# Performance work log

Measured on AMD Instinct MI355X. Metric: run time of the kernel, lower is better.

Reference implementation:

```python
import jax, jax.numpy as jnp
import numpy as np
import math

D, NH, NL, NP = 256, 8, 3, 4
HD = D // NH
SPATIAL = ((128, 128), (64, 64), (32, 32))  # static value_spatial_shapes, one (h,w) per level


def _offset_bias():
    # replicates _reset_parameters grid init for sampling_offsets.bias
    thetas = jnp.arange(NH, dtype=jnp.float32) * (2.0 * math.pi / NH)
    grid = jnp.stack([jnp.cos(thetas), jnp.sin(thetas)], -1)  # (NH, 2)
    grid = grid[:, None, None, :] * (jnp.arange(NP, dtype=jnp.float32) + 1.0)[None, None, :, None]
    return jnp.broadcast_to(grid, (NH, NL, NP, 2)).reshape(-1)  # (NH*NL*NP*2,)


def setup_inputs() -> dict:
    key = jax.random.key(0)
    k = jax.random.split(key, 7)
    bs, Lq = 4, 8192
    Lv = sum(h * w for h, w in SPATIAL)  # 21504
    s = 0.02
    return {
        "query": jax.random.normal(k[0], (bs, Lq, D), jnp.float32),
        "reference_points": jax.random.uniform(k[1], (bs, Lq, 4), jnp.float32),
        "value": jax.random.normal(k[2], (bs, Lv, D), jnp.float32),
        "W_off": jax.random.normal(k[3], (D, NH * NL * NP * 2), jnp.float32) * 0.001,
        "b_off": _offset_bias(),
        "W_attn": jax.random.normal(k[4], (D, NH * NL * NP), jnp.float32) * s,
        "b_attn": jnp.zeros((NH * NL * NP,), jnp.float32),
        "W_v": jax.random.normal(k[5], (D, D), jnp.float32) * s,
        "b_v": jnp.zeros((D,), jnp.float32),
        "W_out": jax.random.normal(k[6], (D, D), jnp.float32) * s,
        "b_out": jnp.zeros((D,), jnp.float32),
    }


def _bilinear(vflat, h, w, gx, gy):
    # F.grid_sample(mode='bilinear', align_corners=False, padding_mode='zeros')
    # vflat: (B, C, h*w); gx, gy: (B, P) in [-1, 1] -> (B, C, P)
    x = ((gx + 1.0) * w - 1.0) * 0.5
    y = ((gy + 1.0) * h - 1.0) * 0.5
    x0f = jnp.floor(x); y0f = jnp.floor(y)
    wx1 = x - x0f; wy1 = y - y0f
    x0 = x0f.astype(jnp.int32); y0 = y0f.astype(jnp.int32)

    def gather(xi, yi, wgt):
        valid = (xi >= 0) & (xi < w) & (yi >= 0) & (yi < h)
        idx = jnp.clip(yi, 0, h - 1) * w + jnp.clip(xi, 0, w - 1)
        g = jnp.take_along_axis(vflat, idx[:, None, :], axis=2)  # (B, C, P)
        return g * (wgt * valid)[:, None, :]

    return (gather(x0, y0, (1.0 - wx1) * (1.0 - wy1))
            + gather(x0 + 1, y0, wx1 * (1.0 - wy1))
            + gather(x0, y0 + 1, (1.0 - wx1) * wy1)
            + gather(x0 + 1, y0 + 1, wx1 * wy1))


def reference(query, reference_points, value, W_off, b_off, W_attn, b_attn, W_v, b_v, W_out, b_out):
    bs, Lq, _ = query.shape
    v = value @ W_v + b_v                                           # (bs, Lv, D)
    v4 = v.reshape(bs, -1, NH, HD)
    off = (query @ W_off + b_off).reshape(bs, Lq, NH, NL, NP, 2)
    aw = jax.nn.softmax((query @ W_attn + b_attn).reshape(bs, Lq, NH, NL * NP), axis=-1)
    aw = aw.reshape(bs, Lq, NH, NL, NP)
    ref = reference_points[..., :2][:, :, None, None, None, :]      # (bs, Lq, 1, 1, 1, 2)
    pts = jnp.clip(ref + off, 0.0, 1.0)                             # (bs, Lq, NH, NL, NP, 2)

    out = jnp.zeros((bs, Lq, NH, HD), query.dtype)
    start = 0
    for lvl, (h, w) in enumerate(SPATIAL):
        # faithful to torch source: (bs, NH, h*w, HD) reinterpreted row-major as (bs*NH, HD, h, w)
        v_lvl = v4[:, start:start + h * w].transpose(0, 2, 1, 3).reshape(bs * NH, HD, h * w)
        g = pts[:, :, :, lvl].transpose(0, 2, 1, 3, 4).reshape(bs * NH, Lq * NP, 2) * 2.0 - 1.0
        sampled = _bilinear(v_lvl, h, w, g[..., 0], g[..., 1]).reshape(bs, NH, HD, Lq, NP)
        out = out + jnp.einsum('bhdqp,bhqp->bqhd', sampled, aw[:, :, :, lvl].transpose(0, 2, 1, 3))
        start += h * w

    return out.reshape(bs, Lq, D) @ W_out + b_out
```

## Files before the change

kernel.cpp:

```cpp
#include <hip/hip_runtime.h>
#include <math.h>

#define LV 21504
#define LQ 8192
#define BS 4
#define NHD 8
#define HD 32
#define DIM 256

typedef __attribute__((ext_vector_type(4))) float f32x4;
typedef __attribute__((ext_vector_type(8))) short s16x8;
typedef unsigned short ushort_t;
typedef unsigned int uint_t;

__device__ __forceinline__ void bsplit(float f, ushort_t& h, ushort_t& l) {
  uint_t u = __float_as_uint(f);
  uint_t hr = (u + 0x7fffu + ((u >> 16) & 1u)) >> 16;
  h = (ushort_t)hr;
  float fh = __uint_as_float(hr << 16);
  float fl = f - fh;
  uint_t v = __float_as_uint(fl);
  l = (ushort_t)((v + 0x7fffu + ((v >> 16) & 1u)) >> 16);
}

__device__ __forceinline__ uint_t bf16rne(float f) {
  uint_t u = __float_as_uint(f);
  return (u + 0x7fffu + ((u >> 16) & 1u)) >> 16;
}

__global__ __launch_bounds__(256) void k_wsplit(
    const float* __restrict__ Wv, const float* __restrict__ Woff,
    const float* __restrict__ Wattn, ushort_t* __restrict__ wbuf)
{
  int c = blockIdx.x;
  int k = threadIdx.x;
  float w;
  ushort_t *dh, *dl;
  if (c < 256) {
    w = Wv[(size_t)k * 256 + c];
    dh = wbuf + (size_t)c * 256 + k;
    dl = wbuf + 65536 + (size_t)c * 256 + k;
  } else {
    int co = c - 256;
    w = (co < 192) ? Woff[(size_t)k * 192 + co] : Wattn[(size_t)k * 96 + (co - 192)];
    dh = wbuf + 131072 + (size_t)co * 256 + k;
    dl = wbuf + 204800 + (size_t)co * 256 + k;
  }
  ushort_t h, l;
  bsplit(w, h, l);
  *dh = h; *dl = l;
}

__global__ __launch_bounds__(256) void k_wsplit2(
    const float* __restrict__ Wout, ushort_t* __restrict__ tb)
{
  int c = blockIdx.x;
  int k = threadIdx.x;
  float w = Wout[(size_t)k * 256 + c];
  ushort_t h, l;
  bsplit(w, h, l);
  tb[(size_t)c * 256 + k] = h;
  tb[65536 + (size_t)c * 256 + k] = l;
}

__global__ __launch_bounds__(256, 3) void k_vproj(
    const float* __restrict__ value, const ushort_t* __restrict__ wbuf,
    const float* __restrict__ bv, ushort_t* __restrict__ vvb)
{
  __shared__ ushort_t lA[2][2][64][72];

  int bid = blockIdx.x;
  int b = bid / 336, rem = bid % 336;
  int l, mp;
  if (rem < 256)      { l = 0; mp = rem; }
  else if (rem < 320) { l = 1; mp = rem - 256; }
  else                { l = 2; mp = rem - 320; }
  const int startl[3] = {0, 16384, 20480};
  const int hwd[3]    = {512, 128, 32};
  int start = startl[l], hd32 = hwd[l], m0 = mp * 2;

  int t = threadIdx.x;
  int wave = t >> 6, lane = t & 63;
  int l15 = lane & 15, l4 = lane >> 4;
  int n0 = wave * 64;

  const float* Ab = value + (size_t)b * LV * DIM;
  int r0s = t >> 4, kq = t & 15;
  const float* aptr[4];
  #pragma unroll
  for (int j = 0; j < 4; ++j) {
    int row = r0s + 16 * j;
    aptr[j] = Ab + (size_t)(start + (row & 31) * hd32 + m0 + (row >> 5)) * DIM + kq * 4;
  }

  f32x4 acc[4][4];
  #pragma unroll
  for (int m = 0; m < 4; ++m)
    #pragma unroll
    for (int n = 0; n < 4; ++n) acc[m][n] = (f32x4){0.f, 0.f, 0.f, 0.f};

  float4 pf[4];
  #pragma unroll
  for (int j = 0; j < 4; ++j) pf[j] = *(const float4*)(aptr[j]);

  #pragma unroll
  for (int j = 0; j < 4; ++j) {
    int row = r0s + 16 * j;
    float a[4] = {pf[j].x, pf[j].y, pf[j].z, pf[j].w};
    ushort_t hh[4], ll[4];
    #pragma unroll
    for (int q = 0; q < 4; ++q) bsplit(a[q], hh[q], ll[q]);
    uint2 uh, ul;
    uh.x = (uint_t)hh[0] | ((uint_t)hh[1] << 16);
    uh.y = (uint_t)hh[2] | ((uint_t)hh[3] << 16);
    ul.x = (uint_t)ll[0] | ((uint_t)ll[1] << 16);
    ul.y = (uint_t)ll[2] | ((uint_t)ll[3] << 16);
    *(uint2*)&lA[0][0][row][kq * 4] = uh;
    *(uint2*)&lA[0][1][row][kq * 4] = ul;
  }
  __syncthreads();

  int cur = 0;
  for (int s = 0; s < 4; ++s) {
    if (s < 3) {
      #pragma unroll
      for (int j = 0; j < 4; ++j) pf[j] = *(const float4*)(aptr[j] + (s + 1) * 64);
    }
    #pragma unroll
    for (int c = 0; c < 2; ++c) {
      int k0 = s * 64 + c * 32;
      s16x8 bh[4], bl[4];
      #pragma unroll
      for (int n = 0; n < 4; ++n) {
        int col = n0 + n * 16 + l15;
        bh[n] = *(const s16x8*)(wbuf + (size_t)col * 256 + k0 + l4 * 8);
        bl[n] = *(const s16x8*)(wbuf + 65536 + (size_t)col * 256 + k0 + l4 * 8);
      }
      s16x8 ah[4], al[4];
      #pragma unroll
      for (int m = 0; m < 4; ++m) {
        ah[m] = *(const s16x8*)&lA[cur][0][m * 16 + l15][c * 32 + l4 * 8];
        al[m] = *(const s16x8*)&lA[cur][1][m * 16 + l15][c * 32 + l4 * 8];
      }
      #pragma unroll
      for (int n = 0; n < 4; ++n)
        #pragma unroll
        for (int m = 0; m < 4; ++m) {
          acc[m][n] = __builtin_amdgcn_mfma_f32_16x16x32_bf16(ah[m], bh[n], acc[m][n], 0, 0, 0);
          acc[m][n] = __builtin_amdgcn_mfma_f32_16x16x32_bf16(al[m], bh[n], acc[m][n], 0, 0, 0);
          acc[m][n] = __builtin_amdgcn_mfma_f32_16x16x32_bf16(ah[m], bl[n], acc[m][n], 0, 0, 0);
        }
    }
    if (s < 3) {
      #pragma unroll
      for (int j = 0; j < 4; ++j) {
        int row = r0s + 16 * j;
        float a[4] = {pf[j].x, pf[j].y, pf[j].z, pf[j].w};
        ushort_t hh[4], ll[4];
        #pragma unroll
        for (int q = 0; q < 4; ++q) bsplit(a[q], hh[q], ll[q]);
        uint2 uh, ul;
        uh.x = (uint_t)hh[0] | ((uint_t)hh[1] << 16);
        uh.y = (uint_t)hh[2] | ((uint_t)hh[3] << 16);
        ul.x = (uint_t)ll[0] | ((uint_t)ll[1] << 16);
        ul.y = (uint_t)ll[2] | ((uint_t)ll[3] << 16);
        *(uint2*)&lA[cur ^ 1][0][row][kq * 4] = uh;
        *(uint2*)&lA[cur ^ 1][1][row][kq * 4] = ul;
      }
    }
    __syncthreads();
    cur ^= 1;
  }

  #pragma unroll
  for (int m = 0; m < 4; ++m) {
    int d = (m & 1) * 16 + l4 * 4;
    int mloc = m0 + (m >> 1);
    #pragma unroll
    for (int n = 0; n < 4; ++n) {
      int col = n0 + n * 16 + l15;
      int g = col >> 5, j = col & 31;
      float bias = bv[col];
      f32x4 o = acc[m][n];
      uint_t h0 = bf16rne(o[0] + bias), h1 = bf16rne(o[1] + bias);
      uint_t h2 = bf16rne(o[2] + bias), h3 = bf16rne(o[3] + bias);
      uint2 pk;
      pk.x = h0 | (h1 << 16);
      pk.y = h2 | (h3 << 16);
      ushort_t* dst = vvb + (((size_t)(b * NHD + g) * LV + start + (size_t)mloc * 32 + j) * 32 + d);
      *(uint2*)dst = pk;
    }
  }
}

__global__ __launch_bounds__(384, 3) void k_offattn(
    const float* __restrict__ query, const ushort_t* __restrict__ wbuf,
    const float* __restrict__ boff, const float* __restrict__ battn,
    float* __restrict__ offattn)
{
  __shared__ ushort_t lAh[64][40];
  __shared__ ushort_t lAl[64][40];
  int r0 = blockIdx.x * 64;
  int t = threadIdx.x;
  int wave = t >> 6, lane = t & 63;
  int l15 = lane & 15, l4 = lane >> 4;
  int n0 = wave * 48;
  const ushort_t* wh = wbuf + 131072;
  const ushort_t* wl = wbuf + 204800;

  f32x4 acc[4][3];
  #pragma unroll
  for (int m = 0; m < 4; ++m)
    #pragma unroll
    for (int n = 0; n < 3; ++n) acc[m][n] = (f32x4){0.f, 0.f, 0.f, 0.f};

  for (int s = 0; s < 8; ++s) {
    int k0 = s * 32;
    s16x8 bh[3], bl[3];
    #pragma unroll
    for (int n = 0; n < 3; ++n) {
      int col = n0 + n * 16 + l15;
      bh[n] = *(const s16x8*)(wh + (size_t)col * 256 + k0 + l4 * 8);
      bl[n] = *(const s16x8*)(wl + (size_t)col * 256 + k0 + l4 * 8);
    }
    #pragma unroll
    for (int i = 0; i < 2; ++i) {
      int u = i * 384 + t;
      if (u < 512) {
        int row = u >> 3, kq = u & 7;
        float4 v = *(const float4*)(query + (size_t)(r0 + row) * DIM + k0 + kq * 4);
        float a0[4] = {v.x, v.y, v.z, v.w};
        ushort_t hh[4], ll[4];
        #pragma unroll
        for (int j = 0; j < 4; ++j) bsplit(a0[j], hh[j], ll[j]);
        *(uint_t*)&lAh[row][kq * 4]     = (uint_t)hh[0] | ((uint_t)hh[1] << 16);
        *(uint_t*)&lAh[row][kq * 4 + 2] = (uint_t)hh[2] | ((uint_t)hh[3] << 16);
        *(uint_t*)&lAl[row][kq * 4]     = (uint_t)ll[0] | ((uint_t)ll[1] << 16);
        *(uint_t*)&lAl[row][kq * 4 + 2] = (uint_t)ll[2] | ((uint_t)ll[3] << 16);
      }
    }
    __syncthreads();
    s16x8 ah[4], al[4];
    #pragma unroll
    for (int m = 0; m < 4; ++m) {
      ah[m] = *(const s16x8*)&lAh[m * 16 + l15][l4 * 8];
      al[m] = *(const s16x8*)&lAl[m * 16 + l15][l4 * 8];
    }
    #pragma unroll
    for (int n = 0; n < 3; ++n)
      #pragma unroll
      for (int m = 0; m < 4; ++m) {
        acc[m][n] = __builtin_amdgcn_mfma_f32_16x16x32_bf16(ah[m], bh[n], acc[m][n], 0, 0, 0);
        acc[m][n] = __builtin_amdgcn_mfma_f32_16x16x32_bf16(al[m], bh[n], acc[m][n], 0, 0, 0);
        acc[m][n] = __builtin_amdgcn_mfma_f32_16x16x32_bf16(ah[m], bl[n], acc[m][n], 0, 0, 0);
      }
    __syncthreads();
  }
  #pragma unroll
  for (int m = 0; m < 4; ++m)
    #pragma unroll
    for (int n = 0; n < 3; ++n) {
      int col = n0 + n * 16 + l15;
      float bias = (col < 192) ? boff[col] : battn[col - 192];
      #pragma unroll
      for (int i = 0; i < 4; ++i)
        offattn[(size_t)(r0 + m * 16 + l4 * 4 + i) * 288 + col] = acc[m][n][i] + bias;
    }
}

__global__ __launch_bounds__(256) void k_sample(
    const float* __restrict__ offattn, const float* __restrict__ refp,
    const ushort_t* __restrict__ vvb, uint_t* __restrict__ midp)
{
  __shared__ float4 metaw[64][13];
  __shared__ uint4  metaa[64][13];
  __shared__ float  smx[64], sinv[64];

  int t = threadIdx.x;
  int e0 = blockIdx.x * 64;

  {
    int it = t >> 2, j = t & 3;
    int e = e0 + it;
    int n = e & 7, bq = e >> 3;
    const float* lgp = offattn + (size_t)bq * 288 + 192 + n * 12;
    float l0 = lgp[j], l1 = lgp[j + 4], l2 = lgp[j + 8];
    float m = fmaxf(fmaxf(l0, l1), l2);
    m = fmaxf(m, __shfl_xor(m, 1));
    m = fmaxf(m, __shfl_xor(m, 2));
    float s = __expf(l0 - m) + __expf(l1 - m) + __expf(l2 - m);
    s += __shfl_xor(s, 1);
    s += __shfl_xor(s, 2);
    if (j == 0) { smx[it] = m; sinv[it] = 1.f / s; }
  }
  __syncthreads();

  const int startl[3] = {0, 16384, 20480};
  const int whl[3]    = {128, 64, 32};
  #pragma unroll
  for (int r = 0; r < 3; ++r) {
    int task = r * 256 + t;
    int it = task / 12, p = task % 12;
    int e = e0 + it;
    int n = e & 7, bq = e >> 3;
    int l = p >> 2;
    int w = whl[l], h = w;
    float fw = (float)w;
    const float* oa = offattn + (size_t)bq * 288;
    float ox = oa[n * 24 + p * 2], oy = oa[n * 24 + p * 2 + 1];
    float lg = oa[192 + n * 12 + p];
    float aw = __expf(lg - smx[it]) * sinv[it];
    float rx = refp[bq * 4], ry = refp[bq * 4 + 1];
    float px = fminf(fmaxf(rx + ox, 0.f), 1.f);
    float py = fminf(fmaxf(ry + oy, 0.f), 1.f);
    float x = px * fw - 0.5f, y = py * fw - 0.5f;
    float x0f = floorf(x), y0f = floorf(y);
    int x0 = (int)x0f, y0 = (int)y0f;
    float wx1 = x - x0f, wy1 = y - y0f;
    float wx0 = 1.f - wx1, wy0 = 1.f - wy1;
    float vx0 = ((uint_t)x0 < (uint_t)w) ? 1.f : 0.f;
    float vx1 = ((uint_t)(x0 + 1) < (uint_t)w) ? 1.f : 0.f;
    float vy0 = ((uint_t)y0 < (uint_t)h) ? 1.f : 0.f;
    float vy1 = ((uint_t)(y0 + 1) < (uint_t)h) ? 1.f : 0.f;
    int xc0 = min(max(x0, 0), w - 1), xc1 = min(max(x0 + 1, 0), w - 1);
    int yc0 = min(max(y0, 0), h - 1), yc1 = min(max(y0 + 1, 0), h - 1);
    int s0 = startl[l];
    uint4 av;
    av.x = (uint_t)(s0 + yc0 * w + xc0) * 64u;
    av.y = (uint_t)(s0 + yc0 * w + xc1) * 64u;
    av.z = (uint_t)(s0 + yc1 * w + xc0) * 64u;
    av.w = (uint_t)(s0 + yc1 * w + xc1) * 64u;
    float4 wv;
    wv.x = aw * wy0 * wx0 * vy0 * vx0;
    wv.y = aw * wy0 * wx1 * vy0 * vx1;
    wv.z = aw * wy1 * wx0 * vy1 * vx0;
    wv.w = aw * wy1 * wx1 * vy1 * vx1;
    metaw[it][p] = wv;
    metaa[it][p] = av;
  }
  __syncthreads();

  #pragma unroll
  for (int r = 0; r < 2; ++r) {
    int it = (t >> 3) + r * 32;
    int c4 = t & 7;
    int e = e0 + it;
    int n = e & 7, bq = e >> 3, b = bq >> 13;
    const char* vb = (const char*)vvb + (size_t)(b * NHD + n) * LV * 64 + c4 * 8;
    f32x4 acc = (f32x4){0.f, 0.f, 0.f, 0.f};
    #pragma unroll
    for (int p = 0; p < 12; ++p) {
      float4 wv = metaw[it][p];
      uint4  av = metaa[it][p];
      uint2 g00 = *(const uint2*)(vb + av.x);
      uint2 g01 = *(const uint2*)(vb + av.y);
      uint2 g10 = *(const uint2*)(vb + av.z);
      uint2 g11 = *(const uint2*)(vb + av.w);
      f32x4 f;
      f[0] = __uint_as_float(g00.x << 16); f[1] = __uint_as_float(g00.x & 0xffff0000u);
      f[2] = __uint_as_float(g00.y << 16); f[3] = __uint_as_float(g00.y & 0xffff0000u);
      acc += wv.x * f;
      f[0] = __uint_as_float(g01.x << 16); f[1] = __uint_as_float(g01.x & 0xffff0000u);
      f[2] = __uint_as_float(g01.y << 16); f[3] = __uint_as_float(g01.y & 0xffff0000u);
      acc += wv.y * f;
      f[0] = __uint_as_float(g10.x << 16); f[1] = __uint_as_float(g10.x & 0xffff0000u);
      f[2] = __uint_as_float(g10.y << 16); f[3] = __uint_as_float(g10.y & 0xffff0000u);
      acc += wv.z * f;
      f[0] = __uint_as_float(g11.x << 16); f[1] = __uint_as_float(g11.x & 0xffff0000u);
      f[2] = __uint_as_float(g11.y << 16); f[3] = __uint_as_float(g11.y & 0xffff0000u);
      acc += wv.w * f;
    }
    uint4 pk;
    ushort_t h16, l16;
    bsplit(acc[0], h16, l16); pk.x = (uint_t)h16 | ((uint_t)l16 << 16);
    bsplit(acc[1], h16, l16); pk.y = (uint_t)h16 | ((uint_t)l16 << 16);
    bsplit(acc[2], h16, l16); pk.z = (uint_t)h16 | ((uint_t)l16 << 16);
    bsplit(acc[3], h16, l16); pk.w = (uint_t)h16 | ((uint_t)l16 << 16);
    *(uint4*)(midp + (size_t)bq * 256 + n * 32 + c4 * 4) = pk;
  }
}

__global__ __launch_bounds__(256, 3) void k_out(
    const uint_t* __restrict__ midp, const ushort_t* __restrict__ wtb,
    const float* __restrict__ bout, float* __restrict__ out)
{
  __shared__ ushort_t lAh[64][40];
  __shared__ ushort_t lAl[64][40];
  int r0 = blockIdx.x * 64;
  int t = threadIdx.x;
  int wave = t >> 6, lane = t & 63;
  int l15 = lane & 15, l4 = lane >> 4;
  int n0 = wave * 64;

  f32x4 acc[4][4];
  #pragma unroll
  for (int m = 0; m < 4; ++m)
    #pragma unroll
    for (int n = 0; n < 4; ++n) acc[m][n] = (f32x4){0.f, 0.f, 0.f, 0.f};

  for (int s = 0; s < 8; ++s) {
    int k0 = s * 32;
    s16x8 bh[4], bl[4];
    #pragma unroll
    for (int n = 0; n < 4; ++n) {
      int col = n0 + n * 16 + l15;
      bh[n] = *(const s16x8*)(wtb + (size_t)col * 256 + k0 + l4 * 8);
      bl[n] = *(const s16x8*)(wtb + 65536 + (size_t)col * 256 + k0 + l4 * 8);
    }
    #pragma unroll
    for (int i = 0; i < 2; ++i) {
      int u = i * 256 + t;
      int row = u >> 3, kq = u & 7;
      uint4 v = *(const uint4*)(midp + (size_t)(r0 + row) * DIM + k0 + kq * 4);
      uint_t a0 = v.x, a1 = v.y, a2 = v.z, a3 = v.w;
      *(uint_t*)&lAh[row][kq * 4]     = (a0 & 0xffffu) | ((a1 & 0xffffu) << 16);
      *(uint_t*)&lAh[row][kq * 4 + 2] = (a2 & 0xffffu) | ((a3 & 0xffffu) << 16);
      *(uint_t*)&lAl[row][kq * 4]     = (a0 >> 16) | (a1 & 0xffff0000u);
      *(uint_t*)&lAl[row][kq * 4 + 2] = (a2 >> 16) | (a3 & 0xffff0000u);
    }
    __syncthreads();
    s16x8 ah[4], al[4];
    #pragma unroll
    for (int m = 0; m < 4; ++m) {
      ah[m] = *(const s16x8*)&lAh[m * 16 + l15][l4 * 8];
      al[m] = *(const s16x8*)&lAl[m * 16 + l15][l4 * 8];
    }
    #pragma unroll
    for (int n = 0; n < 4; ++n)
      #pragma unroll
      for (int m = 0; m < 4; ++m) {
        acc[m][n] = __builtin_amdgcn_mfma_f32_16x16x32_bf16(ah[m], bh[n], acc[m][n], 0, 0, 0);
        acc[m][n] = __builtin_amdgcn_mfma_f32_16x16x32_bf16(al[m], bh[n], acc[m][n], 0, 0, 0);
        acc[m][n] = __builtin_amdgcn_mfma_f32_16x16x32_bf16(ah[m], bl[n], acc[m][n], 0, 0, 0);
      }
    __syncthreads();
  }
  #pragma unroll
  for (int m = 0; m < 4; ++m)
    #pragma unroll
    for (int n = 0; n < 4; ++n) {
      int col = n0 + n * 16 + l15;
      float bias = bout[col];
      #pragma unroll
      for (int i = 0; i < 4; ++i)
        out[(size_t)(r0 + m * 16 + l4 * 4 + i) * DIM + col] = acc[m][n][i] + bias;
    }
}

extern "C" void kernel_launch(void* const* d_in, const int* in_sizes, int n_in,
                              void* d_out, int out_size, void* d_ws, size_t ws_size,
                              hipStream_t stream) {
  const float* query = (const float*)d_in[0];
  const float* refp  = (const float*)d_in[1];
  const float* value = (const float*)d_in[2];
  const float* Woff  = (const float*)d_in[3];
  const float* boff  = (const float*)d_in[4];
  const float* Wattn = (const float*)d_in[5];
  const float* battn = (const float*)d_in[6];
  const float* Wv    = (const float*)d_in[7];
  const float* bv    = (const float*)d_in[8];
  const float* Wout  = (const float*)d_in[9];
  const float* bout  = (const float*)d_in[10];
  float* out = (float*)d_out;
  ushort_t* wbuf = (ushort_t*)d_out;

  float* ws      = (float*)d_ws;
  ushort_t* vvb  = (ushort_t*)ws;
  float* offattn = ws + 22020096;
  uint_t* midp   = (uint_t*)(ws + 22020096 + 9437184);
  ushort_t* wtb  = (ushort_t*)ws;

  hipLaunchKernelGGL(k_wsplit,  dim3(544),   dim3(256), 0, stream, Wv, Woff, Wattn, wbuf);
  hipLaunchKernelGGL(k_vproj,   dim3(1344),  dim3(256), 0, stream, value, wbuf, bv, vvb);
  hipLaunchKernelGGL(k_offattn, dim3(512),   dim3(384), 0, stream, query, wbuf, boff, battn, offattn);
  hipLaunchKernelGGL(k_sample,  dim3(4096),  dim3(256), 0, stream, offattn, refp, vvb, midp);
  hipLaunchKernelGGL(k_wsplit2, dim3(256),   dim3(256), 0, stream, Wout, wtb);
  hipLaunchKernelGGL(k_out,     dim3(512),   dim3(256), 0, stream, midp, wtb, bout, out);
}
```

Measured before the change: 342.2 us.

## Split vproj N across 8 waves and drop LDS double buffering

The value-projection kernel now runs 512 threads (8 waves), each wave computing a 64x32 output slice instead of 64x64. Accumulator and B-fragment register use per wave is halved, and the launch bound asks for 4 blocks per CU. The LDS A tile is single-buffered, so an extra barrier is needed between compute and refilling. Weight fragments are loaded once per 64-wide k step. The goal is higher occupancy and more latency hiding, at the cost of more synchronisation and less overlap between loads and MFMA work.

```diff
diff --git a/kernel.cpp b/kernel.cpp
--- a/kernel.cpp
+++ b/kernel.cpp
@@ -63,11 +63,11 @@
   tb[65536 + (size_t)c * 256 + k] = l;
 }
 
-__global__ __launch_bounds__(256, 3) void k_vproj(
+__global__ __launch_bounds__(512, 4) void k_vproj(
     const float* __restrict__ value, const ushort_t* __restrict__ wbuf,
     const float* __restrict__ bv, ushort_t* __restrict__ vvb)
 {
-  __shared__ ushort_t lA[2][2][64][72];
+  __shared__ ushort_t lA[2][64][72];
 
   int bid = blockIdx.x;
   int b = bid / 336, rem = bid % 336;
@@ -82,113 +82,121 @@
   int t = threadIdx.x;
   int wave = t >> 6, lane = t & 63;
   int l15 = lane & 15, l4 = lane >> 4;
-  int n0 = wave * 64;
-
-  const float* Ab = value + (size_t)b * LV * DIM;
-  int r0s = t >> 4, kq = t & 15;
-  const float* aptr[4];
-  #pragma unroll
-  for (int j = 0; j < 4; ++j) {
-    int row = r0s + 16 * j;
-    aptr[j] = Ab + (size_t)(start + (row & 31) * hd32 + m0 + (row >> 5)) * DIM + kq * 4;
-  }
-
-  f32x4 acc[4][4];
+  int n0 = wave * 32;
+
+  int srow = t >> 3, kq = t & 7;
+  const float* ap = value + (size_t)b * LV * DIM
+                  + (size_t)(start + (srow & 31) * hd32 + m0 + (srow >> 5)) * DIM + kq * 4;
+
+  f32x4 acc[4][2];
   #pragma unroll
   for (int m = 0; m < 4; ++m)
     #pragma unroll
-    for (int n = 0; n < 4; ++n) acc[m][n] = (f32x4){0.f, 0.f, 0.f, 0.f};
-
-  float4 pf[4];
-  #pragma unroll
-  for (int j = 0; j < 4; ++j) pf[j] = *(const float4*)(aptr[j]);
-
-  #pragma unroll
-  for (int j = 0; j < 4; ++j) {
-    int row = r0s + 16 * j;
-    float a[4] = {pf[j].x, pf[j].y, pf[j].z, pf[j].w};
+    for (int n = 0; n < 2; ++n) acc[m][n] = (f32x4){0.f, 0.f, 0.f, 0.f};
+
+  {
+    float4 p0 = *(const float4*)(ap);
+    float4 p1 = *(const float4*)(ap + 32);
+    float a0[4] = {p0.x, p0.y, p0.z, p0.w};
+    float a1[4] = {p1.x, p1.y, p1.z, p1.w};
     ushort_t hh[4], ll[4];
-    #pragma unroll
-    for (int q = 0; q < 4; ++q) bsplit(a[q], hh[q], ll[q]);
     uint2 uh, ul;
+    #pragma unroll
+    for (int q = 0; q < 4; ++q) bsplit(a0[q], hh[q], ll[q]);
     uh.x = (uint_t)hh[0] | ((uint_t)hh[1] << 16);
     uh.y = (uint_t)hh[2] | ((uint_t)hh[3] << 16);
     ul.x = (uint_t)ll[0] | ((uint_t)ll[1] << 16);
     ul.y = (uint_t)ll[2] | ((uint_t)ll[3] << 16);
-    *(uint2*)&lA[0][0][row][kq * 4] = uh;
-    *(uint2*)&lA[0][1][row][kq * 4] = ul;
+    *(uint2*)&lA[0][srow][kq * 4] = uh;
+    *(uint2*)&lA[1][srow][kq * 4] = ul;
+    #pragma unroll
+    for (int q = 0; q < 4; ++q) bsplit(a1[q], hh[q], ll[q]);
+    uh.x = (uint_t)hh[0] | ((uint_t)hh[1] << 16);
+    uh.y = (uint_t)hh[2] | ((uint_t)hh[3] << 16);
+    ul.x = (uint_t)ll[0] | ((uint_t)ll[1] << 16);
+    ul.y = (uint_t)ll[2] | ((uint_t)ll[3] << 16);
+    *(uint2*)&lA[0][srow][32 + kq * 4] = uh;
+    *(uint2*)&lA[1][srow][32 + kq * 4] = ul;
   }
   __syncthreads();
 
-  int cur = 0;
   for (int s = 0; s < 4; ++s) {
+    int k0 = s * 64;
+    s16x8 bh[2][2], bl[2][2];
+    #pragma unroll
+    for (int c = 0; c < 2; ++c)
+      #pragma unroll
+      for (int n = 0; n < 2; ++n) {
+        int col = n0 + n * 16 + l15;
+        int kk = k0 + c * 32 + l4 * 8;
+        bh[c][n] = *(const s16x8*)(wbuf + (size_t)col * 256 + kk);
+        bl[c][n] = *(const s16x8*)(wbuf + 65536 + (size_t)col * 256 + kk);
+      }
+    float4 p0, p1;
     if (s < 3) {
-      #pragma unroll
-      for (int j = 0; j < 4; ++j) pf[j] = *(const float4*)(aptr[j] + (s + 1) * 64);
+      p0 = *(const float4*)(ap + (s + 1) * 64);
+      p1 = *(const float4*)(ap + (s + 1) * 64 + 32);
     }
     #pragma unroll
     for (int c = 0; c < 2; ++c) {
-      int k0 = s * 64 + c * 32;
-      s16x8 bh[4], bl[4];
-      #pragma unroll
-      for (int n = 0; n < 4; ++n) {
-        int col = n0 + n * 16 + l15;
-        bh[n] = *(const s16x8*)(wbuf + (size_t)col * 256 + k0 + l4 * 8);
-        bl[n] = *(const s16x8*)(wbuf + 65536 + (size_t)col * 256 + k0 + l4 * 8);
+      s16x8 ah[4], al[4];
+      #pragma unroll
+      for (int m = 0; m < 4; ++m) {
+        ah[m] = *(const s16x8*)&lA[0][m * 16 + l15][c * 32 + l4 * 8];
+        al[m] = *(const s16x8*)&lA[1][m * 16 + l15][c * 32 + l4 * 8];
       }
-      s16x8 ah[4], al[4];
-      #pragma unroll
-      for (int m = 0; m < 4; ++m) {
-        ah[m] = *(const s16x8*)&lA[cur][0][m * 16 + l15][c * 32 + l4 * 8];
-        al[m] = *(const s16x8*)&lA[cur][1][m * 16 + l15][c * 32 + l4 * 8];
-      }
-      #pragma unroll
-      for (int n = 0; n < 4; ++n)
+      #pragma unroll
+      for (int n = 0; n < 2; ++n)
         #pragma unroll
         for (int m = 0; m < 4; ++m) {
-          acc[m][n] = __builtin_amdgcn_mfma_f32_16x16x32_bf16(ah[m], bh[n], acc[m][n], 0, 0, 0);
-          acc[m][n] = __builtin_amdgcn_mfma_f32_16x16x32_bf16(al[m], bh[n], acc[m][n], 0, 0, 0);
-          acc[m][n] = __builtin_amdgcn_mfma_f32_16x16x32_bf16(ah[m], bl[n], acc[m][n], 0, 0, 0);
+          acc[m][n] = __builtin_amdgcn_mfma_f32_16x16x32_bf16(ah[m], bh[c][n], acc[m][n], 0, 0, 0);
+          acc[m][n] = __builtin_amdgcn_mfma_f32_16x16x32_bf16(al[m], bh[c][n], acc[m][n], 0, 0, 0);
+          acc[m][n] = __builtin_amdgcn_mfma_f32_16x16x32_bf16(ah[m], bl[c][n], acc[m][n], 0, 0, 0);
         }
     }
+    __syncthreads();
     if (s < 3) {
-      #pragma unroll
-      for (int j = 0; j < 4; ++j) {
-        int row = r0s + 16 * j;
-        float a[4] = {pf[j].x, pf[j].y, pf[j].z, pf[j].w};
-        ushort_t hh[4], ll[4];
-        #pragma unroll
-        for (int q = 0; q < 4; ++q) bsplit(a[q], hh[q], ll[q]);
-        uint2 uh, ul;
-        uh.x = (uint_t)hh[0] | ((uint_t)hh[1] << 16);
-        uh.y = (uint_t)hh[2] | ((uint_t)hh[3] << 16);
-        ul.x = (uint_t)ll[0] | ((uint_t)ll[1] << 16);
-        ul.y = (uint_t)ll[2] | ((uint_t)ll[3] << 16);
-        *(uint2*)&lA[cur ^ 1][0][row][kq * 4] = uh;
-        *(uint2*)&lA[cur ^ 1][1][row][kq * 4] = ul;
-      }
-    }
-    __syncthreads();
-    cur ^= 1;
-  }
-
-  #pragma unroll
-  for (int m = 0; m < 4; ++m) {
-    int d = (m & 1) * 16 + l4 * 4;
-    int mloc = m0 + (m >> 1);
-    #pragma unroll
-    for (int n = 0; n < 4; ++n) {
-      int col = n0 + n * 16 + l15;
-      int g = col >> 5, j = col & 31;
-      float bias = bv[col];
+      float a0[4] = {p0.x, p0.y, p0.z, p0.w};
+      float a1[4] = {p1.x, p1.y, p1.z, p1.w};
+      ushort_t hh[4], ll[4];
+      uint2 uh, ul;
+      #pragma unroll
+      for (int q = 0; q < 4; ++q) bsplit(a0[q], hh[q], ll[q]);
+      uh.x = (uint_t)hh[0] | ((uint_t)hh[1] << 16);
+      uh.y = (uint_t)hh[2] | ((uint_t)hh[3] << 16);
+      ul.x = (uint_t)ll[0] | ((uint_t)ll[1] << 16);
+      ul.y = (uint_t)ll[2] | ((uint_t)ll[3] << 16);
+      *(uint2*)&lA[0][srow][kq * 4] = uh;
+      *(uint2*)&lA[1][srow][kq * 4] = ul;
+      #pragma unroll
+      for (int q = 0; q < 4; ++q) bsplit(a1[q], hh[q], ll[q]);
+      uh.x = (uint_t)hh[0] | ((uint_t)hh[1] << 16);
+      uh.y = (uint_t)hh[2] | ((uint_t)hh[3] << 16);
+      ul.x = (uint_t)ll[0] | ((uint_t)ll[1] << 16);
+      ul.y = (uint_t)ll[2] | ((uint_t)ll[3] << 16);
+      *(uint2*)&lA[0][srow][32 + kq * 4] = uh;
+      *(uint2*)&lA[1][srow][32 + kq * 4] = ul;
+      __syncthreads();
+    }
+  }
+
+  #pragma unroll
+  for (int n = 0; n < 2; ++n) {
+    int col = n0 + n * 16 + l15;
+    int g = col >> 5, j = col & 31;
+    float bias = bv[col];
+    ushort_t* base = vvb + ((size_t)(b * NHD + g) * LV + start) * 32;
+    #pragma unroll
+    for (int m = 0; m < 4; ++m) {
+      int d = (m & 1) * 16 + l4 * 4;
+      int mloc = m0 + (m >> 1);
       f32x4 o = acc[m][n];
       uint_t h0 = bf16rne(o[0] + bias), h1 = bf16rne(o[1] + bias);
       uint_t h2 = bf16rne(o[2] + bias), h3 = bf16rne(o[3] + bias);
       uint2 pk;
       pk.x = h0 | (h1 << 16);
       pk.y = h2 | (h3 << 16);
-      ushort_t* dst = vvb + (((size_t)(b * NHD + g) * LV + start + (size_t)mloc * 32 + j) * 32 + d);
-      *(uint2*)dst = pk;
+      *(uint2*)(base + ((size_t)mloc * 32 + j) * 32 + d) = pk;
     }
   }
 }
@@ -471,7 +479,7 @@
   ushort_t* wtb  = (ushort_t*)ws;
 
   hipLaunchKernelGGL(k_wsplit,  dim3(544),   dim3(256), 0, stream, Wv, Woff, Wattn, wbuf);
-  hipLaunchKernelGGL(k_vproj,   dim3(1344),  dim3(256), 0, stream, value, wbuf, bv, vvb);
+  hipLaunchKernelGGL(k_vproj,   dim3(1344),  dim3(512), 0, stream, value, wbuf, bv, vvb);
   hipLaunchKernelGGL(k_offattn, dim3(512),   dim3(384), 0, stream, query, wbuf, boff, battn, offattn);
   hipLaunchKernelGGL(k_sample,  dim3(4096),  dim3(256), 0, stream, offattn, refp, vvb, midp);
   hipLaunchKernelGGL(k_wsplit2, dim3(256),   dim3(256), 0, stream, Wout, wtb);
```

Result: faster. 334.2 us (-2.3%).
